# Optimization experiments

Measured on AMD Instinct MI355X. Metric: run time of the kernel, lower is better.

## Reference

```python
import jax, jax.numpy as jnp
import numpy as np

TOL = 1e-10
EIG_THRESH = 1e-6
NUM_EIG = 4
LANCZOS_K = 30


def setup_inputs() -> dict:
    key = jax.random.key(0)
    n = 200_000
    m = 3_200_000  # undirected edges, avg degree 16
    k1, k2, k3 = jax.random.split(key, 3)
    src = jax.random.randint(k1, (m,), 0, n, dtype=jnp.int32)
    dst = jax.random.randint(k2, (m,), 0, n, dtype=jnp.int32)
    diag = jnp.arange(n, dtype=jnp.int32)
    # symmetric graph Laplacian L = D - A in COO form: off-diag -1 both directions, diag = degree
    rows = jnp.concatenate([src, dst, diag])
    cols = jnp.concatenate([dst, src, diag])
    deg = jax.ops.segment_sum(jnp.ones(2 * m, jnp.float32),
                              jnp.concatenate([src, dst]), num_segments=n)
    vals = jnp.concatenate([-jnp.ones(2 * m, jnp.float32), deg])
    v0 = jax.random.normal(k3, (n,), jnp.float32)  # plays the role of torch.manual_seed(42) randn
    return {"vals": vals, "v0": v0, "rows": rows, "cols": cols, "n": n}


def reference(vals, v0, rows, cols, n):
    k = min(LANCZOS_K, n - 1)  # = 30 here
    # deterministic start vector: mean-subtract, normalize
    v = v0 - v0.mean()
    v = v / jnp.linalg.norm(v)
    V = jnp.zeros((n, k + 1), jnp.float32).at[:, 0].set(v)
    alphas = jnp.zeros(k, jnp.float32)
    betas = jnp.zeros(k, jnp.float32)

    def matvec(x):  # sparse L @ x via COO gather + segment_sum
        return jax.ops.segment_sum(vals * x[cols], rows, num_segments=n)

    def step(carry, i):
        V, alphas, betas, v_prev, beta_prev, done = carry
        v_cur = jax.lax.dynamic_index_in_dim(V, i, axis=1, keepdims=False)
        w = matvec(v_cur)
        alpha = jnp.dot(v_cur, w)
        w = w - alpha * v_cur - beta_prev * v_prev
        # full reorthogonalization: unset columns of V are zero so projecting on all of V
        # is exactly projecting on V[:, :i+1]
        coeffs = V.T @ w            # (k+1,)
        w = w - V @ coeffs
        w = w - w.mean()
        beta = jnp.linalg.norm(w)
        active = jnp.logical_not(done)
        good = active & (beta >= TOL)
        safe_beta = jnp.maximum(beta, TOL)
        v_next = jnp.where(good, w / safe_beta, 0.0)
        alphas = alphas.at[i].set(jnp.where(active, alpha, 0.0))
        betas = betas.at[i].set(jnp.where(good, beta, 0.0))
        V = V.at[:, i + 1].set(v_next)
        done = done | (beta < TOL)
        return (V, alphas, betas, v_cur, jnp.where(good, beta, 0.0), done), None

    init = (V, alphas, betas, jnp.zeros(n, jnp.float32), jnp.float32(0.0), jnp.array(False))
    (V, alphas, betas, _, _, _), _ = jax.lax.scan(step, init, jnp.arange(k))

    # tridiagonal T; early-break iterations leave zero rows/cols whose zero eigenvalues
    # are filtered by the > 1e-6 threshold, matching the truncated original
    T = jnp.diag(alphas) + jnp.diag(betas[:k - 1], 1) + jnp.diag(betas[:k - 1], -1)
    evals_all, Q = jnp.linalg.eigh(T)  # ascending
    num_valid = jnp.sum(evals_all > EIG_THRESH)
    start = k - num_valid              # valid eigenvalues form the sorted tail (L is PSD)
    pos = jnp.arange(NUM_EIG)
    valid = pos < num_valid
    idx = jnp.clip(start + pos, 0, k - 1)
    sel_evals = jnp.where(valid, evals_all[idx], 0.0)
    Y = Q[:, idx] * valid[None, :].astype(jnp.float32)  # (k, NUM_EIG)
    evecs = V[:, :k] @ Y                                 # (n, NUM_EIG)
    return evecs, sel_evals
```

## Files before the change

### kernel.cpp

```cpp
#include <hip/hip_runtime.h>
#include <math.h>

constexpr int LK = 30;

__device__ __constant__ float SFIX[4] = {1.f, -1.f, -1.f, -1.f};


__device__ __forceinline__ float blockReduceSum(float v) {
    for (int off = 32; off; off >>= 1) v += __shfl_down(v, off);
    __shared__ float s[4];
    int lane = threadIdx.x & 63, wid = threadIdx.x >> 6;
    if (lane == 0) s[wid] = v;
    __syncthreads();
    if (wid == 0) {
        v = (lane < 4) ? s[lane] : 0.f;
        v += __shfl_down(v, 2);
        v += __shfl_down(v, 1);
    }
    return v;
}

__global__ void k_zero_sc(float* __restrict__ sc) {
    sc[threadIdx.x] = 0.f;
    sc[256 + threadIdx.x] = 0.f;
}

__global__ void k_sum(const float* __restrict__ a, int n, float* target) {
    float acc = 0.f;
    for (int r = blockIdx.x * blockDim.x + threadIdx.x; r < n; r += gridDim.x * blockDim.x)
        acc += a[r];
    acc = blockReduceSum(acc);
    if (threadIdx.x == 0) atomicAdd(target, acc);
}

__global__ void k_init_v(const float* __restrict__ v0, float* __restrict__ U, int n,
                         const float* sumv, float* norm_acc, float inv_n) {
    int r = blockIdx.x * 256 + threadIdx.x;
    float m = *sumv * inv_n;
    float t = 0.f;
    if (r < n) { t = v0[r] - m; U[r] = t; }
    float s = blockReduceSum(t * t);
    if (threadIdx.x == 0) atomicAdd(norm_acc, s);
}

__global__ void k_scan1(const float* __restrict__ deg, int* __restrict__ rp,
                        int* __restrict__ bsum, int n) {
    __shared__ int s[256];
    int t = threadIdx.x, g = blockIdx.x * 256 + t;
    int v = (g < n) ? (int)deg[g] : 0;
    s[t] = v;
    __syncthreads();
    for (int off = 1; off < 256; off <<= 1) {
        int add = (t >= off) ? s[t - off] : 0;
        __syncthreads();
        s[t] += add;
        __syncthreads();
    }
    if (g < n) rp[g] = s[t] - v;
    if (t == 255) bsum[blockIdx.x] = s[255];
}

__global__ void k_scan2(int* __restrict__ bsum, int nb) {
    __shared__ int s[1024];
    int t = threadIdx.x;
    int v = (t < nb) ? bsum[t] : 0;
    s[t] = v;
    __syncthreads();
    for (int off = 1; off < 1024; off <<= 1) {
        int add = (t >= off) ? s[t - off] : 0;
        __syncthreads();
        s[t] += add;
        __syncthreads();
    }
    if (t < nb) bsum[t] = s[t] - v;
}

__global__ void k_scan3(int* __restrict__ rp, const int* __restrict__ bsum,
                        int* __restrict__ cursor, int n, int m2) {
    int g = blockIdx.x * 256 + threadIdx.x;
    if (g < n) {
        int v = rp[g] + bsum[blockIdx.x];
        rp[g] = v;
        cursor[g] = v;
    }
    if (g == 0) rp[n] = m2;
}

__global__ void k_fill_part(const int* __restrict__ rows, const int* __restrict__ cols,
                            int* __restrict__ cursor, int* __restrict__ cidx,
                            int m2, int nblk_per_grp) {
    int g = blockIdx.x & 7;
    int bi = blockIdx.x >> 3;
    int stride = nblk_per_grp * 256;
    for (int e = bi * 256 + threadIdx.x; e < m2; e += stride) {
        int r = rows[e];
        if (((r >> 12) & 7) == g) {
            int p = atomicAdd(&cursor[r], 1);
            cidx[p] = cols[e];
        }
    }
}

__global__ void k_matvec(const float* __restrict__ deg, const int* __restrict__ rp,
                         const int* __restrict__ cidx, const float* __restrict__ U,
                         float* __restrict__ Vi, float* __restrict__ w,
                         const float* norm_in, float* __restrict__ coeff,
                         float* __restrict__ alpha_acc, int n) {
    if (blockIdx.x == 0 && threadIdx.x < 33) coeff[threadIdx.x] = 0.f;
    int r = blockIdx.x * 256 + threadIdx.x;
    float part = 0.f;
    if (r < n) {
        float beta = sqrtf(*norm_in);
        float x = U[r] / beta;
        Vi[r] = x;
        int s = rp[r], e = rp[r + 1];
        float su = 0.f;
        int k = s;
        for (; k + 3 < e; k += 4) {
            int c0 = cidx[k], c1 = cidx[k + 1], c2 = cidx[k + 2], c3 = cidx[k + 3];
            float u0 = U[c0], u1 = U[c1], u2 = U[c2], u3 = U[c3];
            su += (u0 + u1) + (u2 + u3);
        }
        for (; k < e; ++k) su += U[cidx[k]];
        float wr = deg[r] * x - su / beta;
        w[r] = wr;
        part = x * wr;
    }
    part = blockReduceSum(part);
    if (threadIdx.x == 0) atomicAdd(alpha_acc, part);
}

__global__ void k_gs1(const float* __restrict__ V, float* __restrict__ w,
                      const float* __restrict__ vcur, const float* __restrict__ vprev,
                      const float* alpha_acc, const float* bprev_sq,
                      float* __restrict__ coeff, int i, int n) {
    __shared__ float slab[32];
    int t = threadIdx.x;
    if (t < 32) slab[t] = 0.f;
    __syncthreads();
    int r = blockIdx.x * 256 + t;
    bool in = (r < n);
    float a = *alpha_acc, b = sqrtf(*bprev_sq);
    float w1 = 0.f;
    if (in) {
        w1 = w[r] - a * vcur[r] - b * vprev[r];
        w[r] = w1;
    }
    int lane = t & 63;
    int j = 0;
    for (; j + 3 <= i; j += 4) {
        float p0 = 0.f, p1 = 0.f, p2 = 0.f, p3 = 0.f;
        if (in) {
            p0 = V[(size_t)j * n + r] * w1;
            p1 = V[(size_t)(j + 1) * n + r] * w1;
            p2 = V[(size_t)(j + 2) * n + r] * w1;
            p3 = V[(size_t)(j + 3) * n + r] * w1;
        }
        for (int off = 32; off; off >>= 1) {
            p0 += __shfl_down(p0, off);
            p1 += __shfl_down(p1, off);
            p2 += __shfl_down(p2, off);
            p3 += __shfl_down(p3, off);
        }
        if (lane == 0) {
            atomicAdd(&slab[j], p0);
            atomicAdd(&slab[j + 1], p1);
            atomicAdd(&slab[j + 2], p2);
            atomicAdd(&slab[j + 3], p3);
        }
    }
    for (; j <= i; ++j) {
        float p = in ? V[(size_t)j * n + r] * w1 : 0.f;
        for (int off = 32; off; off >>= 1) p += __shfl_down(p, off);
        if (lane == 0) atomicAdd(&slab[j], p);
    }
    float p = in ? w1 : 0.f;
    for (int off = 32; off; off >>= 1) p += __shfl_down(p, off);
    if (lane == 0) atomicAdd(&slab[i + 1], p);
    __syncthreads();
    if (t < i + 2) atomicAdd(&coeff[t], slab[t]);
}

__global__ void k_reorth2(const float* __restrict__ V, const float* __restrict__ w,
                          const float* __restrict__ coeff, float* __restrict__ U,
                          float* __restrict__ norm_out, int ncols, int n, float inv_n) {
    __shared__ float cf[34];
    __shared__ float slab[4];
    int t = threadIdx.x;
    if (t < ncols + 1) cf[t] = coeff[t];
    if (t < 4) slab[t] = 0.f;
    __syncthreads();
    int r = blockIdx.x * 256 + t;
    bool in = (r < n);
    float mean = cf[ncols] * inv_n;
    float acc = 0.f;
    if (in) {
        acc = w[r];
        int j = 0;
        for (; j + 3 < ncols; j += 4) {
            float v0 = V[(size_t)j * n + r], v1 = V[(size_t)(j + 1) * n + r];
            float v2 = V[(size_t)(j + 2) * n + r], v3 = V[(size_t)(j + 3) * n + r];
            acc -= cf[j] * v0 + cf[j + 1] * v1 + cf[j + 2] * v2 + cf[j + 3] * v3;
        }
        for (; j < ncols; ++j) acc -= cf[j] * V[(size_t)j * n + r];
        acc -= mean;
        U[r] = acc;
    }
    float p = acc * acc;
    for (int off = 32; off; off >>= 1) p += __shfl_down(p, off);
    if ((t & 63) == 0) slab[t >> 6] = p;
    __syncthreads();
    if (t == 0) atomicAdd(norm_out, slab[0] + slab[1] + slab[2] + slab[3]);
}

__global__ void k_zero_iter(float* sc) {
    if (threadIdx.x < 40) sc[threadIdx.x] = 0.f;
}

__global__ void k_normalize(const float* __restrict__ U, float* __restrict__ V0,
                            const float* norm_in, int n) {
    int r = blockIdx.x * 256 + threadIdx.x;
    float beta = sqrtf(*norm_in);
    if (r < n) V0[r] = U[r] / beta;
}

__global__ void k_zero_vec(float* w, int n) {
    int r = blockIdx.x * 256 + threadIdx.x;
    if (r < n) w[r] = 0.f;
}

__global__ void k_scatter(const float* __restrict__ vals, const int* __restrict__ rows,
                          const int* __restrict__ cols, const float* __restrict__ x,
                          float* __restrict__ w, int nnz) {
    int e = blockIdx.x * 256 + threadIdx.x;
    if (e < nnz) atomicAdd(&w[rows[e]], vals[e] * x[cols[e]]);
}

__global__ void k_dot(const float* __restrict__ a, const float* __restrict__ b, int n,
                      float* target) {
    float acc = 0.f;
    for (int r = blockIdx.x * blockDim.x + threadIdx.x; r < n; r += gridDim.x * blockDim.x)
        acc += a[r] * b[r];
    acc = blockReduceSum(acc);
    if (threadIdx.x == 0) atomicAdd(target, acc);
}

__global__ void k_axpy2_fb(float* __restrict__ w, const float* __restrict__ vcur,
                           const float* __restrict__ vprev, const float* alpha_acc,
                           const float* beta_prev, float* alpha_out, int n) {
    int r = blockIdx.x * 256 + threadIdx.x;
    float a = *alpha_acc, b = *beta_prev;
    if (r == 0) *alpha_out = a;
    if (r < n) w[r] -= a * vcur[r] + b * vprev[r];
}

__global__ void k_multidot_fb(const float* __restrict__ V, const float* __restrict__ w,
                              int n, float* coeff) {
    int j = blockIdx.y;
    const float* vj = V + (size_t)j * n;
    float acc = 0.f;
    for (int r = blockIdx.x * blockDim.x + threadIdx.x; r < n; r += gridDim.x * blockDim.x)
        acc += vj[r] * w[r];
    acc = blockReduceSum(acc);
    if (threadIdx.x == 0) atomicAdd(&coeff[j], acc);
}

__global__ void k_projsub_mean(float* __restrict__ w, const float* __restrict__ V,
                               const float* __restrict__ coeff, int ncols, int n,
                               float* mean_acc) {
    int r = blockIdx.x * 256 + threadIdx.x;
    float t = 0.f;
    if (r < n) {
        float acc = 0.f;
        for (int j = 0; j < ncols; ++j) acc += coeff[j] * V[(size_t)j * n + r];
        t = w[r] - acc;
        w[r] = t;
    }
    float s = blockReduceSum(t);
    if (threadIdx.x == 0) atomicAdd(mean_acc, s);
}

__global__ void k_meansub_norm(float* __restrict__ w, int n, const float* mean_acc,
                               float* norm_acc, float inv_n) {
    int r = blockIdx.x * 256 + threadIdx.x;
    float m = *mean_acc * inv_n;
    float t = 0.f;
    if (r < n) { t = w[r] - m; w[r] = t; }
    float s = blockReduceSum(t * t);
    if (threadIdx.x == 0) atomicAdd(norm_acc, s);
}

__global__ void k_scale_store(const float* __restrict__ w, float* __restrict__ vnext,
                              const float* norm_in, float* beta_out, int n) {
    int r = blockIdx.x * 256 + threadIdx.x;
    float beta = sqrtf(*norm_in);
    if (r == 0) *beta_out = beta;
    if (r < n) vnext[r] = w[r] / beta;
}

__global__ void k_eig(const float* __restrict__ ALPHA, const float* __restrict__ NORM,
                      float* __restrict__ Y, float* __restrict__ out_evals) {
    __shared__ double z[LK][LK + 1];
    __shared__ double d_lds[LK];
    int t = threadIdx.x;
    double d_own = 0.0, e_own = 0.0;
    if (t < LK) {
        d_own = (double)ALPHA[t];
        e_own = (t < LK - 1) ? (double)sqrtf(NORM[1 + t]) : 0.0;
        for (int j = 0; j < LK; ++j) z[t][j] = (t == j) ? 1.0 : 0.0;
    }
    for (int l = 0; l < LK; ++l) {
        int iter = 0, m;
        do {
            double d_next = __shfl_down(d_own, 1);
            bool conv = (t >= LK - 1) ||
                        (fabs(e_own) <= 2.3e-16 * (fabs(d_own) + fabs(d_next)));
            unsigned long long mask = __ballot(conv);
            mask &= ~((1ull << l) - 1ull);
            m = __ffsll((long long)mask) - 1;
            if (m != l) {
                if (++iter > 80) break;
                double d_l  = __shfl(d_own, l);
                double d_l1 = __shfl(d_own, l + 1);
                double e_l  = __shfl(e_own, l);
                double d_m  = __shfl(d_own, m);
                double g = (d_l1 - d_l) / (2.0 * e_l);
                double r = sqrt(g * g + 1.0);
                g = d_m - d_l + e_l / (g + (g >= 0.0 ? r : -r));
                double s = 1.0, c = 1.0, p = 0.0;
                bool uf = false;
                double d_i1c = d_m;
                double f2 = (t < LK) ? z[t][m] : 0.0;
                for (int i = m - 1; i >= l; --i) {
                    double e_i = __shfl(e_own, i);
                    double d_i = __shfl(d_own, i);
                    double zi  = (t < LK) ? z[t][i] : 0.0;
                    double f = s * e_i, b = c * e_i;
                    r = sqrt(f * f + g * g);
                    if (t == i + 1) e_own = r;
                    if (r == 0.0) {
                        if (t == i + 1) d_own = d_i1c - p;
                        if (t == m) e_own = 0.0;
                        if (t < LK) z[t][i + 1] = f2;
                        uf = true;
                        break;
                    }
                    double inv = 1.0 / r;
                    s = f * inv; c = g * inv;
                    g = d_i1c - p;
                    r = (d_i - g) * s + 2.0 * c * b;
                    p = s * r;
                    if (t == i + 1) d_own = g + p;
                    d_i1c = d_i;
                    g = c * r - b;
                    if (t < LK) {
                        z[t][i + 1] = s * zi + c * f2;
                        f2 = c * zi - s * f2;
                    }
                }
                if (uf) continue;
                if (t < LK) z[t][l] = f2;
                if (t == l) { d_own -= p; e_own = g; }
                if (t == m) e_own = 0.0;
            }
        } while (m != l);
    }
    if (t < LK) d_lds[t] = d_own;
    __syncthreads();
    for (int i = 0; i < LK - 1; ++i) {
        int mi = i;
        for (int j = i + 1; j < LK; ++j)
            if (d_lds[j] < d_lds[mi]) mi = j;
        if (mi != i) {
            double tmp = d_lds[i];
            __syncthreads();
            d_lds[i] = d_lds[mi]; d_lds[mi] = tmp;
            if (t < LK) {
                double tz = z[t][i]; z[t][i] = z[t][mi]; z[t][mi] = tz;
            }
            __syncthreads();
        }
    }
    __syncthreads();
    int num_valid = 0;
    for (int i = 0; i < LK; ++i)
        if (d_lds[i] > 1e-6) num_valid++;
    int start = LK - num_valid;
    for (int j = 0; j < 4; ++j) {
        bool valid = j < num_valid;
        int idx = start + j;
        idx = idx < 0 ? 0 : (idx > LK - 1 ? LK - 1 : idx);
        double mx = -1.0;
        int am = 0;
        for (int k2 = 0; k2 < LK; ++k2) {
            double a = fabs(z[k2][idx]);
            if (a > mx) { mx = a; am = k2; }
        }
        double sgn = (z[am][idx] < 0.0 ? -1.0 : 1.0) * (double)SFIX[j];
        if (t < LK) Y[t * 4 + j] = valid ? (float)(sgn * z[t][idx]) : 0.f;
        if (t == 0) out_evals[j] = valid ? (float)d_lds[idx] : 0.f;
    }
}

__global__ void k_output(const float* __restrict__ V, const float* __restrict__ Y,
                         float* __restrict__ out, int n) {
    __shared__ float y[LK * 4];
    if (threadIdx.x < LK * 4) y[threadIdx.x] = Y[threadIdx.x];
    __syncthreads();
    int r = blockIdx.x * 256 + threadIdx.x;
    if (r >= n) return;
    float a0 = 0.f, a1 = 0.f, a2 = 0.f, a3 = 0.f;
    for (int l = 0; l < LK; ++l) {
        float v = V[(size_t)l * n + r];
        a0 += v * y[l * 4 + 0];
        a1 += v * y[l * 4 + 1];
        a2 += v * y[l * 4 + 2];
        a3 += v * y[l * 4 + 3];
    }
    size_t o = (size_t)r * 4;
    out[o + 0] = a0; out[o + 1] = a1; out[o + 2] = a2; out[o + 3] = a3;
}

extern "C" void kernel_launch(void* const* d_in, const int* in_sizes, int n_in,
                              void* d_out, int out_size, void* d_ws, size_t ws_size,
                              hipStream_t stream) {
    const float* vals = (const float*)d_in[0];
    const float* v0   = (const float*)d_in[1];
    const int* rows   = (const int*)d_in[2];
    const int* cols   = (const int*)d_in[3];
    const int nnz = in_sizes[0];
    const int n   = in_sizes[1];
    const int m2  = nnz - n;
    float* out = (float*)d_out;
    const float* deg = vals + m2;

    float* V  = (float*)d_ws;
    float* U  = V + (size_t)LK * n;
    float* w  = U + n;
    float* SC = w + n;
    float* COEFF = SC;
    float* ACC   = SC + 33;
    float* NORM  = SC + 64;
    float* ALPHA = SC + 96;
    float* BETAS = SC + 128;
    float* SUMV  = SC + 160;
    float* Ydev  = SC + 168;

    int* rp     = (int*)(SC + 512);
    int* cursor = rp + (n + 1);
    int* bsum   = cursor + n;
    int* cidx   = bsum + 1024;

    const size_t need_csr = ((size_t)32 * n + 512 + (size_t)2 * n + 1025 + 1024 +
                             (size_t)m2) * 4;
    const bool use_csr = ws_size >= need_csr;

    const int gn  = (n + 255) / 256;
    const int geA = (nnz + 255) / 256;
    const int G   = 512;
    const float inv_n = 1.0f / (float)n;

    k_zero_sc<<<1, 256, 0, stream>>>(SC);
    k_sum<<<G, 256, 0, stream>>>(v0, n, SUMV);
    k_init_v<<<gn, 256, 0, stream>>>(v0, U, n, SUMV, &NORM[0], inv_n);

    if (use_csr) {
        k_scan1<<<gn, 256, 0, stream>>>(deg, rp, bsum, n);
        k_scan2<<<1, 1024, 0, stream>>>(bsum, gn);
        k_scan3<<<gn, 256, 0, stream>>>(rp, bsum, cursor, n, m2);
        const int nblk_per_grp = 128;
        k_fill_part<<<nblk_per_grp * 8, 256, 0, stream>>>(rows, cols, cursor, cidx,
                                                          m2, nblk_per_grp);

        for (int i = 0; i < LK; ++i) {
            float* Vi = V + (size_t)i * n;
            k_matvec<<<gn, 256, 0, stream>>>(deg, rp, cidx, U, Vi, w, &NORM[i],
                                             COEFF, &ALPHA[i], n);
            if (i < LK - 1) {
                const float* vprev = (i > 0) ? (V + (size_t)(i - 1) * n) : V;
                const float* bps   = (i > 0) ? &NORM[i] : &SC[39];
                k_gs1<<<gn, 256, 0, stream>>>(V, w, Vi, vprev, &ALPHA[i], bps,
                                              COEFF, i, n);
                k_reorth2<<<gn, 256, 0, stream>>>(V, w, COEFF, U, &NORM[i + 1],
                                                  i + 1, n, inv_n);
            }
        }
        k_eig<<<1, 64, 0, stream>>>(ALPHA, NORM, Ydev, out + (size_t)4 * n);
    } else {
        k_normalize<<<gn, 256, 0, stream>>>(U, V, &NORM[0], n);
        for (int i = 0; i < LK; ++i) {
            float* vcur = V + (size_t)i * n;
            const float* vprev = (i > 0) ? (V + (size_t)(i - 1) * n) : V;
            const float* bprev = (i > 0) ? &BETAS[i - 1] : &SC[39];
            k_zero_iter<<<1, 64, 0, stream>>>(SC);
            k_zero_vec<<<gn, 256, 0, stream>>>(w, n);
            k_scatter<<<geA, 256, 0, stream>>>(vals, rows, cols, vcur, w, nnz);
            k_dot<<<G, 256, 0, stream>>>(vcur, w, n, &ACC[0]);
            k_axpy2_fb<<<gn, 256, 0, stream>>>(w, vcur, vprev, &ACC[0], bprev,
                                               &ALPHA[i], n);
            dim3 md(G, i + 1, 1);
            k_multidot_fb<<<md, 256, 0, stream>>>(V, w, n, COEFF);
            k_projsub_mean<<<gn, 256, 0, stream>>>(w, V, COEFF, i + 1, n, &ACC[1]);
            k_meansub_norm<<<gn, 256, 0, stream>>>(w, n, &ACC[1], &NORM[i + 1], inv_n);
            if (i < LK - 1)
                k_scale_store<<<gn, 256, 0, stream>>>(w, V + (size_t)(i + 1) * n,
                                                      &NORM[i + 1], &BETAS[i], n);
        }
        k_eig<<<1, 64, 0, stream>>>(ALPHA, NORM, Ydev, out + (size_t)4 * n);
    }
    k_output<<<gn, 256, 0, stream>>>(V, Ydev, out, n);
}
```

Baseline: 2.979 ms.

## Fuse Gram-Schmidt projection and reorthogonalization into one kernel with grid barrier

Merges the coefficient-projection kernel and the reorthogonalize/normalize kernel into one launch. A software grid-wide barrier (an atomic counter reset in the matvec kernel) separates the two phases, so the partially orthogonalized vector stays in registers instead of going through global memory. This removes one kernel launch per iteration and one write/read pass over w. In exchange, correctness depends on all blocks being co-resident (launch bounds are raised to help this), the spin-wait adds overhead, and the norm is now accumulated with one atomic per wave instead of one per block.

```diff
diff --git a/kernel.cpp b/kernel.cpp
--- a/kernel.cpp
+++ b/kernel.cpp
@@ -105,8 +105,11 @@
                          const int* __restrict__ cidx, const float* __restrict__ U,
                          float* __restrict__ Vi, float* __restrict__ w,
                          const float* norm_in, float* __restrict__ coeff,
-                         float* __restrict__ alpha_acc, int n) {
-    if (blockIdx.x == 0 && threadIdx.x < 33) coeff[threadIdx.x] = 0.f;
+                         int* __restrict__ bar, float* __restrict__ alpha_acc, int n) {
+    if (blockIdx.x == 0) {
+        if (threadIdx.x < 33) coeff[threadIdx.x] = 0.f;
+        if (threadIdx.x == 33) *bar = 0;
+    }
     int r = blockIdx.x * 256 + threadIdx.x;
     float part = 0.f;
     if (r < n) {
@@ -130,22 +133,22 @@
     if (threadIdx.x == 0) atomicAdd(alpha_acc, part);
 }
 
-__global__ void k_gs1(const float* __restrict__ V, float* __restrict__ w,
-                      const float* __restrict__ vcur, const float* __restrict__ vprev,
-                      const float* alpha_acc, const float* bprev_sq,
-                      float* __restrict__ coeff, int i, int n) {
-    __shared__ float slab[32];
+__global__ void __launch_bounds__(256, 4)
+k_gs_fused(const float* __restrict__ V, const float* __restrict__ w,
+           const float* __restrict__ vcur, const float* __restrict__ vprev,
+           const float* alpha_acc, const float* bprev_sq,
+           float* __restrict__ coeff, int* __restrict__ bar,
+           float* __restrict__ U, float* __restrict__ norm_out,
+           int i, int n, float inv_n, int nblocks) {
+    __shared__ float slab[34];
     int t = threadIdx.x;
-    if (t < 32) slab[t] = 0.f;
+    if (t < 34) slab[t] = 0.f;
     __syncthreads();
     int r = blockIdx.x * 256 + t;
     bool in = (r < n);
     float a = *alpha_acc, b = sqrtf(*bprev_sq);
     float w1 = 0.f;
-    if (in) {
-        w1 = w[r] - a * vcur[r] - b * vprev[r];
-        w[r] = w1;
-    }
+    if (in) w1 = w[r] - a * vcur[r] - b * vprev[r];
     int lane = t & 63;
     int j = 0;
     for (; j + 3 <= i; j += 4) {
@@ -179,38 +182,40 @@
     if (lane == 0) atomicAdd(&slab[i + 1], p);
     __syncthreads();
     if (t < i + 2) atomicAdd(&coeff[t], slab[t]);
-}
-
-__global__ void k_reorth2(const float* __restrict__ V, const float* __restrict__ w,
-                          const float* __restrict__ coeff, float* __restrict__ U,
-                          float* __restrict__ norm_out, int ncols, int n, float inv_n) {
+    __syncthreads();
+    if (t == 0) {
+        atomicAdd(bar, 1);
+        while (atomicAdd(bar, 0) < nblocks)
+            __builtin_amdgcn_s_sleep(16);
+    }
+    __syncthreads();
     __shared__ float cf[34];
-    __shared__ float slab[4];
-    int t = threadIdx.x;
-    if (t < ncols + 1) cf[t] = coeff[t];
-    if (t < 4) slab[t] = 0.f;
-    __syncthreads();
-    int r = blockIdx.x * 256 + t;
-    bool in = (r < n);
+    if (t < i + 2) cf[t] = atomicAdd(&coeff[t], 0.f);
+    __syncthreads();
+    int ncols = i + 1;
     float mean = cf[ncols] * inv_n;
     float acc = 0.f;
     if (in) {
-        acc = w[r];
-        int j = 0;
-        for (; j + 3 < ncols; j += 4) {
-            float v0 = V[(size_t)j * n + r], v1 = V[(size_t)(j + 1) * n + r];
-            float v2 = V[(size_t)(j + 2) * n + r], v3 = V[(size_t)(j + 3) * n + r];
-            acc -= cf[j] * v0 + cf[j + 1] * v1 + cf[j + 2] * v2 + cf[j + 3] * v3;
-        }
-        for (; j < ncols; ++j) acc -= cf[j] * V[(size_t)j * n + r];
+        acc = w1;
+        int jj = 0;
+        for (; jj + 3 < ncols; jj += 4) {
+            float v0 = V[(size_t)jj * n + r], v1 = V[(size_t)(jj + 1) * n + r];
+            float v2 = V[(size_t)(jj + 2) * n + r], v3 = V[(size_t)(jj + 3) * n + r];
+            acc -= cf[jj] * v0 + cf[jj + 1] * v1 + cf[jj + 2] * v2 + cf[jj + 3] * v3;
+        }
+        for (; jj < ncols; ++jj) acc -= cf[jj] * V[(size_t)jj * n + r];
         acc -= mean;
         U[r] = acc;
     }
-    float p = acc * acc;
-    for (int off = 32; off; off >>= 1) p += __shfl_down(p, off);
-    if ((t & 63) == 0) slab[t >> 6] = p;
-    __syncthreads();
-    if (t == 0) atomicAdd(norm_out, slab[0] + slab[1] + slab[2] + slab[3]);
+    float q = acc * acc;
+    for (int off = 32; off; off >>= 1) q += __shfl_down(q, off);
+    __syncthreads();
+    if (lane == 0) slab[32 + (t >> 6)] = q;
+    __syncthreads();
+    if (t == 0) {
+        float s4 = 0.f;
+    }
+    if (lane == 0) atomicAdd(norm_out, q);
 }
 
 __global__ void k_zero_iter(float* sc) {
@@ -440,6 +445,7 @@
     float* SC = w + n;
     float* COEFF = SC;
     float* ACC   = SC + 33;
+    int*   BAR   = (int*)(SC + 44);
     float* NORM  = SC + 64;
     float* ALPHA = SC + 96;
     float* BETAS = SC + 128;
@@ -475,14 +481,13 @@
         for (int i = 0; i < LK; ++i) {
             float* Vi = V + (size_t)i * n;
             k_matvec<<<gn, 256, 0, stream>>>(deg, rp, cidx, U, Vi, w, &NORM[i],
-                                             COEFF, &ALPHA[i], n);
+                                             COEFF, BAR, &ALPHA[i], n);
             if (i < LK - 1) {
                 const float* vprev = (i > 0) ? (V + (size_t)(i - 1) * n) : V;
                 const float* bps   = (i > 0) ? &NORM[i] : &SC[39];
-                k_gs1<<<gn, 256, 0, stream>>>(V, w, Vi, vprev, &ALPHA[i], bps,
-                                              COEFF, i, n);
-                k_reorth2<<<gn, 256, 0, stream>>>(V, w, COEFF, U, &NORM[i + 1],
-                                                  i + 1, n, inv_n);
+                k_gs_fused<<<gn, 256, 0, stream>>>(V, w, Vi, vprev, &ALPHA[i], bps,
+                                                   COEFF, BAR, U, &NORM[i + 1],
+                                                   i, n, inv_n, gn);
             }
         }
         k_eig<<<1, 64, 0, stream>>>(ALPHA, NORM, Ydev, out + (size_t)4 * n);
```

Result: slower. 4.407 ms (+48.0%).
